# Optimization experiments

Hardware: AMD Instinct MI355X
Metric: run time of the kernel (lower is better)

## Reference

```python
import jax, jax.numpy as jnp
import numpy as np

EPS_BN = 1e-4


def gcn_conv(x, W, b, src, dst):
    """PyG GCNConv with added self-loops and symmetric normalization."""
    N = x.shape[0]
    h = x @ W  # [N, out]
    # degree over targets, +1 for the implicit self-loop on every node
    deg = jnp.zeros((N,), x.dtype).at[dst].add(1.0) + 1.0
    dinv = jax.lax.rsqrt(deg)  # deg^{-1/2}
    norm = dinv[src] * dinv[dst]  # per-edge coefficient
    msg = h[src] * norm[:, None]  # [E, out] gather (memory-bound)
    out = jax.ops.segment_sum(msg, dst, num_segments=N)
    out = out + h * (dinv * dinv)[:, None]  # self-loop term, norm = 1/deg
    return out + b


def batch_norm(x, gamma, beta):
    # training-mode BN over the node dim, biased variance (matches torch train)
    m = jnp.mean(x, axis=0)
    v = jnp.mean(jnp.square(x - m), axis=0)
    return (x - m) * jax.lax.rsqrt(v + EPS_BN) * gamma + beta


def setup_inputs() -> dict:
    key = jax.random.key(0)
    ks = jax.random.split(key, 8)
    N, E, D = 100000, 1600000, 64
    L = 2
    x = jax.random.normal(ks[0], (N, D), jnp.float32)
    edge_index = jax.random.randint(ks[1], (2, E), 0, N, jnp.int32)
    batch = jnp.sort(jax.random.randint(ks[2], (N,), 0, 128, jnp.int32))
    s = 1.0 / np.sqrt(D)
    return {
        "x": x,
        "edge_index": edge_index,
        "batch": batch,
        "enc_W": jax.random.normal(ks[3], (L, D, D), jnp.float32) * s,
        "enc_b": jnp.zeros((L, D), jnp.float32),
        "enc_gamma": jnp.ones((L, D), jnp.float32),
        "enc_beta": jnp.zeros((L, D), jnp.float32),
        "attr_W": jax.random.normal(ks[4], (L, D, D), jnp.float32) * s,
        "attr_b": jnp.zeros((L, D), jnp.float32),
        "attr_gamma": jnp.ones((L, D), jnp.float32),
        "attr_beta": jnp.zeros((L, D), jnp.float32),
        "str_W": jax.random.normal(ks[5], (L, D, D), jnp.float32) * s,
        "str_b": jnp.zeros((L, D), jnp.float32),
        "str_gamma": jnp.ones((L, D), jnp.float32),
        "str_beta": jnp.zeros((L, D), jnp.float32),
    }


def reference(x, edge_index, batch, enc_W, enc_b, enc_gamma, enc_beta,
              attr_W, attr_b, attr_gamma, attr_beta,
              str_W, str_b, str_gamma, str_beta):
    src, dst = edge_index[0], edge_index[1]
    L = enc_W.shape[0]

    # ---- Encoder: GCN -> sigmoid -> (dropout id) -> BN ----
    h = x
    for i in range(L):
        h = gcn_conv(h, enc_W[i], enc_b[i], src, dst)
        h = jax.nn.sigmoid(h)
        h = batch_norm(h, enc_gamma[i], enc_beta[i])
    x_enc = h
    # x_pool = global_mean_pool(x_enc, batch) is computed but discarded upstream

    # ---- Attribute decoder: GCN -> (dropout) -> sigmoid (except last) -> BN ----
    h = x_enc
    for i in range(L):
        h = gcn_conv(h, attr_W[i], attr_b[i], src, dst)
        if i != L - 1:
            h = jax.nn.sigmoid(h)
        h = batch_norm(h, attr_gamma[i], attr_beta[i])
    x_att = h

    # ---- Structure decoder ----
    h = x_enc
    for i in range(L):
        h = gcn_conv(h, str_W[i], str_b[i], src, dst)
        if i != L - 1:
            h = jax.nn.sigmoid(h)
        else:
            h = jax.nn.sigmoid(h * 0.5)
        h = batch_norm(h, str_gamma[i], str_beta[i])
    x_str = h

    return (x_str, x_att, x_enc)
```

## Files before the change

kernel.cpp:

```cpp
#include <hip/hip_runtime.h>

#define D 64
#define BCH 4096

typedef __attribute__((ext_vector_type(8))) _Float16 f16x8;
typedef __attribute__((ext_vector_type(4))) float f32x4;

__device__ __forceinline__ float sigmoidf_(float x) {
    return 1.0f / (1.0f + __expf(-x));
}
__device__ __forceinline__ float h2f(ushort u) {
    _Float16 h;
    __builtin_memcpy(&h, &u, 2);
    return (float)h;
}
__device__ __forceinline__ ushort f2h(float f) {
    _Float16 h = (_Float16)f;
    ushort u;
    __builtin_memcpy(&u, &h, 2);
    return u;
}
__device__ __forceinline__ float2 up2(uint v) {
    float2 r;
    r.x = h2f((ushort)(v & 0xffffu));
    r.y = h2f((ushort)(v >> 16));
    return r;
}


__global__ __launch_bounds__(256) void bin_edges(const int* __restrict__ src,
                                                 const int* __restrict__ dst,
                                                 int* __restrict__ bcur,
                                                 uint* __restrict__ bins,
                                                 int CAP, int E) {
    __shared__ uint lp[BCH];
    __shared__ unsigned char lb[BCH];
    __shared__ int hist[128], base[128];
    int t = threadIdx.x;
    int e0 = blockIdx.x * BCH;
    if (t < 128) hist[t] = 0;
    __syncthreads();
    for (int k = t; k < BCH; k += 256) {
        int e = e0 + k;
        uint p = 0xFFFFFFFFu;
        int b = 0;
        if (e < E) {
            int s_ = src[e];
            int d_ = dst[e];
            b = d_ >> 10;
            atomicAdd(&hist[b], 1);
            p = ((uint)s_ << 10) | (uint)(d_ & 1023);
        }
        lp[k] = p;
        lb[k] = (unsigned char)b;
    }
    __syncthreads();
    if (t < 128) {
        int c = hist[t];
        base[t] = (c > 0) ? atomicAdd(&bcur[t], c) : 0;
        hist[t] = 0;
    }
    __syncthreads();
    for (int k = t; k < BCH; k += 256) {
        uint p = lp[k];
        if (p != 0xFFFFFFFFu) {
            int b = lb[k];
            int pos = base[b] + atomicAdd(&hist[b], 1);
            bins[(size_t)b * CAP + pos] = p;
        }
    }
}

__global__ __launch_bounds__(128) void scan_nb(const int* __restrict__ bcur,
                                               int* __restrict__ boff,
                                               int* __restrict__ csr,
                                               int NB, int N, int E) {
    __shared__ int tmp[128];
    int t = threadIdx.x;
    int v = (t < NB) ? bcur[t] : 0;
    tmp[t] = v;
    __syncthreads();
    for (int o = 1; o < 128; o <<= 1) {
        int x = (t >= o) ? tmp[t - o] : 0;
        __syncthreads();
        tmp[t] += x;
        __syncthreads();
    }
    if (t < NB) boff[t] = tmp[t] - v;
    if (t == 0) csr[N] = E;
}

__global__ __launch_bounds__(256) void build_csr(const uint* __restrict__ bins,
                                                 const int* __restrict__ bcur,
                                                 const int* __restrict__ boff,
                                                 int* __restrict__ csr,
                                                 int* __restrict__ sorted,
                                                 float* __restrict__ dinv,
                                                 float* __restrict__ rdinv,
                                                 int CAP, int N) {
    __shared__ int hist[1024];
    __shared__ int part[256];
    int t = threadIdx.x;
    int b = blockIdx.x;
    int nb0 = b << 10;
    int cnt = bcur[b];
    int e0 = boff[b];
    const uint* bp = bins + (size_t)b * CAP;
    for (int k = t; k < 1024; k += 256) hist[k] = 0;
    __syncthreads();
    for (int k = t; k < cnt; k += 256) atomicAdd(&hist[bp[k] & 1023u], 1);
    __syncthreads();
    int v0 = hist[4 * t], v1 = hist[4 * t + 1], v2 = hist[4 * t + 2], v3 = hist[4 * t + 3];
    part[t] = v0 + v1 + v2 + v3;
    __syncthreads();
    for (int o = 1; o < 256; o <<= 1) {
        int x = (t >= o) ? part[t - o] : 0;
        __syncthreads();
        part[t] += x;
        __syncthreads();
    }
    int run = (t > 0) ? part[t - 1] : 0;
    int pre[4];
    pre[0] = run;
    pre[1] = run + v0;
    pre[2] = run + v0 + v1;
    pre[3] = run + v0 + v1 + v2;
    int deg[4] = {v0, v1, v2, v3};
    __syncthreads();
    hist[4 * t + 0] = e0 + pre[0];
    hist[4 * t + 1] = e0 + pre[1];
    hist[4 * t + 2] = e0 + pre[2];
    hist[4 * t + 3] = e0 + pre[3];
#pragma unroll
    for (int j = 0; j < 4; j++) {
        int node = nb0 + 4 * t + j;
        if (node < N) {
            csr[node] = e0 + pre[j];
            float c = (float)deg[j] + 1.0f;
            dinv[node] = rsqrtf(c);
            rdinv[node] = sqrtf(c);
        }
    }
    __syncthreads();
    for (int k = t; k < cnt; k += 256) {
        uint p = bp[k];
        int pos = atomicAdd(&hist[p & 1023u], 1);
        sorted[pos] = (int)(p >> 10);
    }
}


__global__ __launch_bounds__(256) void prep_xd(const float* __restrict__ x,
                                               const float* __restrict__ dinv,
                                               ushort* __restrict__ actd, int N16) {
    int p = blockIdx.x * 256 + threadIdx.x;
    if (p >= N16) return;
    int n = p >> 4;
    float d = dinv[n];
    float4 v = reinterpret_cast<const float4*>(x)[p];
    ushort4 o;
    o.x = f2h(v.x * d);
    o.y = f2h(v.y * d);
    o.z = f2h(v.z * d);
    o.w = f2h(v.w * d);
    reinterpret_cast<ushort4*>(actd)[p] = o;
}

__global__ __launch_bounds__(256) void wprep(const float* __restrict__ W,
                                             ushort* __restrict__ wfrag) {
    int idx = blockIdx.x * 256 + threadIdx.x;
    if (idx >= 4096) return;
    int i = idx & 7;
    int lane = (idx >> 3) & 63;
    int hc = idx >> 9;
    int h = hc >> 2, c = hc & 3;
    int k = h * 32 + (lane >> 4) * 8 + i;
    int j = c * 16 + (lane & 15);
    wfrag[idx] = f2h(W[k * 64 + j]);
}

__global__ __launch_bounds__(256) void layer_prep(const float* __restrict__ ssum,
                                                  const float* __restrict__ sssq,
                                                  const float* __restrict__ gamma,
                                                  const float* __restrict__ beta,
                                                  const float* __restrict__ W,
                                                  float* __restrict__ A,
                                                  float* __restrict__ C,
                                                  float* __restrict__ u,
                                                  ushort* __restrict__ wfrag,
                                                  float invN) {
    __shared__ float As[64], Cs[64];
    int t = threadIdx.x;
    if (t < 64) {
        float m = ssum[t] * invN;
        float var = sssq[t] * invN - m * m;
        float rs = rsqrtf(var + 1e-4f);
        float a = rs * gamma[t];
        As[t] = a;
        A[t] = a;
        float c = fmaf(-m, a, beta[t]);
        Cs[t] = c;
        C[t] = c;
    }
    __syncthreads();
    if (t < 64) {
        float s = 0.f;
        for (int k = 0; k < 64; k++) s = fmaf(Cs[k], W[k * 64 + t], s);
        u[t] = s;
    }
    for (int idx = t; idx < 4096; idx += 256) {
        int i = idx & 7;
        int lane = (idx >> 3) & 63;
        int hc = idx >> 9;
        int h = hc >> 2, c = hc & 3;
        int k = h * 32 + (lane >> 4) * 8 + i;
        int j = c * 16 + (lane & 15);
        wfrag[idx] = f2h(W[k * 64 + j] * As[k]);
    }
}

__global__ __launch_bounds__(64) void finalize_aff(const float* __restrict__ ssum,
                                                   const float* __restrict__ sssq,
                                                   const float* __restrict__ gamma,
                                                   const float* __restrict__ beta,
                                                   float* __restrict__ A,
                                                   float* __restrict__ C, float invN) {
    int c = threadIdx.x;
    float m = ssum[c] * invN;
    float var = sssq[c] * invN - m * m;
    float rs = rsqrtf(var + 1e-4f);
    float a = rs * gamma[c];
    A[c] = a;
    C[c] = fmaf(-m, a, beta[c]);
}


__global__ __launch_bounds__(256) void agg_g(const ushort* __restrict__ actd,
                                             const int* __restrict__ ptr,
                                             const int* __restrict__ srcs,
                                             const float* __restrict__ dinv,
                                             const float* __restrict__ rdinv,
                                             ushort* __restrict__ zh,
                                             float* __restrict__ ssum,
                                             float* __restrict__ sssq,
                                             float* __restrict__ qout, int N, int E) {
    __shared__ float red[2][4][64];
    int lane = threadIdx.x & 63;
    int wv = threadIdx.x >> 6;
    int l7 = lane & 7;
    int Em1 = E - 1;
    const bool do_stats = (ssum != nullptr);
    const bool do_q = (qout != nullptr);
    float ps = 0.f, pq = 0.f;
    int Nh = (N + 1) >> 1;
    for (int n0 = blockIdx.x * 4 + wv; n0 < Nh; n0 += gridDim.x * 4) {
        int nA = n0;
        int nB = n0 + Nh;
        bool hasB = nB < N;
        int sA = ptr[nA], eA = ptr[nA + 1];
        int sB = 0, eB = 0;
        if (hasB) { sB = ptr[nB]; eB = ptr[nB + 1]; }
        float selfA = h2f(actd[((size_t)nA << 6) + lane]);
        float accA = selfA;
        float dnA = dinv[nA];
        float accB = 0.f, dnB = 0.f;
        if (hasB) {
            float selfB = h2f(actd[((size_t)nB << 6) + lane]);
            accB = selfB;
            dnB = dinv[nB];
            if (do_stats) {
                float rb = rdinv[nB];
                float b = selfB * rb;
                ps += b;
                pq += b * b;
            }
        }
        if (do_stats) {
            float ra = rdinv[nA];
            float a = selfA * ra;
            ps += a;
            pq += a * a;
        }
        float qaA = 0.f, qaB = 0.f;
        int iA = sA, iB = sB;
        int idxA = srcs[min(iA + l7, Em1)];
        int idxB = hasB ? srcs[min(iB + l7, Em1)] : 0;
        while (iA + 8 <= eA || iB + 8 <= eB) {
            bool gA = iA + 8 <= eA;
            bool gB = iB + 8 <= eB;
            ushort ua[8], ub[8];
            if (gA) {
#pragma unroll
                for (int j = 0; j < 8; j++) {
                    int u = __builtin_amdgcn_readlane(idxA, j);
                    ua[j] = actd[((size_t)u << 6) + lane];
                    if (do_q) qaA += dinv[u];
                }
            }
            if (gB) {
#pragma unroll
                for (int j = 0; j < 8; j++) {
                    int u = __builtin_amdgcn_readlane(idxB, j);
                    ub[j] = actd[((size_t)u << 6) + lane];
                    if (do_q) qaB += dinv[u];
                }
            }
            int idxA2 = idxA, idxB2 = idxB;
            if (gA) idxA2 = srcs[min(iA + 8 + l7, Em1)];
            if (gB) idxB2 = srcs[min(iB + 8 + l7, Em1)];
            if (gA) {
                accA += ((h2f(ua[0]) + h2f(ua[1])) + (h2f(ua[2]) + h2f(ua[3]))) +
                        ((h2f(ua[4]) + h2f(ua[5])) + (h2f(ua[6]) + h2f(ua[7])));
                iA += 8;
                idxA = idxA2;
            }
            if (gB) {
                accB += ((h2f(ub[0]) + h2f(ub[1])) + (h2f(ub[2]) + h2f(ub[3]))) +
                        ((h2f(ub[4]) + h2f(ub[5])) + (h2f(ub[6]) + h2f(ub[7])));
                iB += 8;
                idxB = idxB2;
            }
        }
        if (iA < eA) {
#pragma unroll
            for (int j = 0; j < 8; j++) {
                int u = __builtin_amdgcn_readlane(idxA, j);
                float w = (iA + j < eA) ? 1.0f : 0.0f;
                float f = h2f(actd[((size_t)u << 6) + lane]);
                accA = fmaf(w, f, accA);
                if (do_q) qaA = fmaf(w, dinv[u], qaA);
            }
        }
        if (hasB && iB < eB) {
#pragma unroll
            for (int j = 0; j < 8; j++) {
                int u = __builtin_amdgcn_readlane(idxB, j);
                float w = (iB + j < eB) ? 1.0f : 0.0f;
                float f = h2f(actd[((size_t)u << 6) + lane]);
                accB = fmaf(w, f, accB);
                if (do_q) qaB = fmaf(w, dinv[u], qaB);
            }
        }
        if (do_q && lane == 0) {
            qout[nA] = dnA * (dnA + qaA);
            if (hasB) qout[nB] = dnB * (dnB + qaB);
        }
        zh[((size_t)nA << 6) + lane] = f2h(accA * dnA);
        if (hasB) zh[((size_t)nB << 6) + lane] = f2h(accB * dnB);
    }
    if (do_stats) {
        red[0][wv][lane] = ps;
        red[1][wv][lane] = pq;
        __syncthreads();
        if (wv == 0) {
            float t0 = red[0][0][lane] + red[0][1][lane] + red[0][2][lane] + red[0][3][lane];
            float t1 = red[1][0][lane] + red[1][1][lane] + red[1][2][lane] + red[1][3][lane];
            atomicAdd(&ssum[lane], t0);
            atomicAdd(&sssq[lane], t1);
        }
    }
}

__global__ __launch_bounds__(256) void agg_dual(const ushort* __restrict__ ab,
                                                const int* __restrict__ ptr,
                                                const int* __restrict__ srcs,
                                                const float* __restrict__ dinv,
                                                const float* __restrict__ rdinv,
                                                ushort* __restrict__ zab,
                                                float* __restrict__ ssA,
                                                float* __restrict__ sqA,
                                                float* __restrict__ ssS,
                                                float* __restrict__ sqS,
                                                int N, int E) {
    __shared__ float red[2][4][128];
    int lane = threadIdx.x & 63;
    int wv = threadIdx.x >> 6;
    int l7 = lane & 7;
    int Em1 = E - 1;
    float2 ps = make_float2(0.f, 0.f), pq = make_float2(0.f, 0.f);
    int Nh = (N + 1) >> 1;
    for (int n0 = blockIdx.x * 4 + wv; n0 < Nh; n0 += gridDim.x * 4) {
        int nA = n0;
        int nB = n0 + Nh;
        bool hasB = nB < N;
        int sA = ptr[nA], eA = ptr[nA + 1];
        int sB = 0, eB = 0;
        if (hasB) { sB = ptr[nB]; eB = ptr[nB + 1]; }
        uint suA = *reinterpret_cast<const uint*>(ab + ((size_t)nA << 7) + (lane << 1));
        float2 accA = up2(suA);
        float dnA = dinv[nA];
        {
            float r = rdinv[nA];
            float ax = accA.x * r, ay = accA.y * r;
            ps.x += ax; ps.y += ay;
            pq.x += ax * ax; pq.y += ay * ay;
        }
        float2 accB = make_float2(0.f, 0.f);
        float dnB = 0.f;
        if (hasB) {
            uint suB = *reinterpret_cast<const uint*>(ab + ((size_t)nB << 7) + (lane << 1));
            accB = up2(suB);
            dnB = dinv[nB];
            float r = rdinv[nB];
            float ax = accB.x * r, ay = accB.y * r;
            ps.x += ax; ps.y += ay;
            pq.x += ax * ax; pq.y += ay * ay;
        }
        int iA = sA, iB = sB;
        int idxA = srcs[min(iA + l7, Em1)];
        int idxB = hasB ? srcs[min(iB + l7, Em1)] : 0;
        while (iA + 8 <= eA || iB + 8 <= eB) {
            bool gA = iA + 8 <= eA;
            bool gB = iB + 8 <= eB;
            uint va[8], vb[8];
            if (gA) {
#pragma unroll
                for (int j = 0; j < 8; j++) {
                    int u = __builtin_amdgcn_readlane(idxA, j);
                    va[j] = *reinterpret_cast<const uint*>(ab + ((size_t)u << 7) + (lane << 1));
                }
            }
            if (gB) {
#pragma unroll
                for (int j = 0; j < 8; j++) {
                    int u = __builtin_amdgcn_readlane(idxB, j);
                    vb[j] = *reinterpret_cast<const uint*>(ab + ((size_t)u << 7) + (lane << 1));
                }
            }
            int idxA2 = idxA, idxB2 = idxB;
            if (gA) idxA2 = srcs[min(iA + 8 + l7, Em1)];
            if (gB) idxB2 = srcs[min(iB + 8 + l7, Em1)];
            if (gA) {
#pragma unroll
                for (int j = 0; j < 8; j++) {
                    float2 f = up2(va[j]);
                    accA.x += f.x;
                    accA.y += f.y;
                }
                iA += 8;
                idxA = idxA2;
            }
            if (gB) {
#pragma unroll
                for (int j = 0; j < 8; j++) {
                    float2 f = up2(vb[j]);
                    accB.x += f.x;
                    accB.y += f.y;
                }
                iB += 8;
                idxB = idxB2;
            }
        }
        if (iA < eA) {
#pragma unroll
            for (int j = 0; j < 8; j++) {
                int u = __builtin_amdgcn_readlane(idxA, j);
                uint v = *reinterpret_cast<const uint*>(ab + ((size_t)u << 7) + (lane << 1));
                float w = (iA + j < eA) ? 1.0f : 0.0f;
                float2 f = up2(v);
                accA.x = fmaf(w, f.x, accA.x);
                accA.y = fmaf(w, f.y, accA.y);
            }
        }
        if (hasB && iB < eB) {
#pragma unroll
            for (int j = 0; j < 8; j++) {
                int u = __builtin_amdgcn_readlane(idxB, j);
                uint v = *reinterpret_cast<const uint*>(ab + ((size_t)u << 7) + (lane << 1));
                float w = (iB + j < eB) ? 1.0f : 0.0f;
                float2 f = up2(v);
                accB.x = fmaf(w, f.x, accB.x);
                accB.y = fmaf(w, f.y, accB.y);
            }
        }
        uint pkA = (uint)f2h(accA.x * dnA) | ((uint)f2h(accA.y * dnA) << 16);
        *reinterpret_cast<uint*>(zab + ((size_t)nA << 7) + (lane << 1)) = pkA;
        if (hasB) {
            uint pkB = (uint)f2h(accB.x * dnB) | ((uint)f2h(accB.y * dnB) << 16);
            *reinterpret_cast<uint*>(zab + ((size_t)nB << 7) + (lane << 1)) = pkB;
        }
    }
    red[0][wv][2 * lane + 0] = ps.x;
    red[0][wv][2 * lane + 1] = ps.y;
    red[1][wv][2 * lane + 0] = pq.x;
    red[1][wv][2 * lane + 1] = pq.y;
    __syncthreads();
    if (wv == 0) {
#pragma unroll
        for (int m0 = 0; m0 < 2; m0++) {
            int m = lane + m0 * 64;
            float t0 = red[0][0][m] + red[0][1][m] + red[0][2][m] + red[0][3][m];
            float t1 = red[1][0][m] + red[1][1][m] + red[1][2][m] + red[1][3][m];
            if (m < 64) {
                atomicAdd(&ssA[m], t0);
                atomicAdd(&sqA[m], t1);
            } else {
                atomicAdd(&ssS[m - 64], t0);
                atomicAdd(&sqS[m - 64], t1);
            }
        }
    }
}

template <int MODE, bool HAS_AFF, int OM>
__global__ __launch_bounds__(256) void gemm_mfma(const ushort* __restrict__ zh, int is,
                                                 const ushort* __restrict__ wfrag,
                                                 const float* __restrict__ bias,
                                                 const float* __restrict__ u,
                                                 const float* __restrict__ q,
                                                 const float* __restrict__ dinv,
                                                 ushort* __restrict__ outh, int os,
                                                 float* __restrict__ outf,
                                                 float* __restrict__ s0,
                                                 float* __restrict__ s1, int N) {
    int tid = threadIdx.x;
    int lane = tid & 63;
    int wv = tid >> 6;
    int l15 = lane & 15;
    int lg = lane >> 4;
    int tb = blockIdx.x * 64;

    const ushort* zrow = zh + (size_t)(tb + wv * 16 + l15) * is + (lg << 3);
    f16x8 a0 = *reinterpret_cast<const f16x8*>(zrow);
    f16x8 a1 = *reinterpret_cast<const f16x8*>(zrow + 32);

    const f16x8* wf = reinterpret_cast<const f16x8*>(wfrag) + lane;

    f32x4 acc[4];
#pragma unroll
    for (int c = 0; c < 4; c++) {
        f32x4 t = {0.f, 0.f, 0.f, 0.f};
        t = __builtin_amdgcn_mfma_f32_16x16x32_f16(a0, wf[(0 * 4 + c) * 64], t, 0, 0, 0);
        t = __builtin_amdgcn_mfma_f32_16x16x32_f16(a1, wf[(1 * 4 + c) * 64], t, 0, 0, 0);
        acc[c] = t;
    }

    int rowbase = tb + wv * 16 + lg * 4;
    float qv[4], dv[4];
    bool vld[4];
#pragma unroll
    for (int r = 0; r < 4; r++) {
        int row = rowbase + r;
        vld[r] = row < N;
        qv[r] = (HAS_AFF && vld[r]) ? q[row] : 0.f;
        dv[r] = (OM == 0 && vld[r]) ? dinv[row] : 0.f;
    }
    float sa[4], sq[4];
#pragma unroll
    for (int c = 0; c < 4; c++) { sa[c] = 0.f; sq[c] = 0.f; }

#pragma unroll
    for (int c = 0; c < 4; c++) {
        int col = c * 16 + l15;
        float bcol = bias[col];
        float ucol = HAS_AFF ? u[col] : 0.f;
        float Acol = (OM == 2) ? s0[col] : 0.f;
        float Ccol = (OM == 2) ? s1[col] : 0.f;
#pragma unroll
        for (int r = 0; r < 4; r++) {
            if (!vld[r]) continue;
            float o = acc[c][r] + bcol;
            if (HAS_AFF) o = fmaf(qv[r], ucol, o);
            float a = (MODE == 0) ? sigmoidf_(o)
                                  : ((MODE == 1) ? o : sigmoidf_(0.5f * o));
            int row = rowbase + r;
            if (OM == 0) {
                outh[(size_t)row * os + col] = f2h(a * dv[r]);
            } else if (OM == 1) {
                sa[c] += a;
                sq[c] += a * a;
            } else {
                outf[((size_t)row << 6) + col] = fmaf(a, Acol, Ccol);
            }
        }
    }

    if (OM == 1) {
        __shared__ float red[2][4][4][16];
#pragma unroll
        for (int c = 0; c < 4; c++) {
            sa[c] += __shfl_xor(sa[c], 16);
            sa[c] += __shfl_xor(sa[c], 32);
            sq[c] += __shfl_xor(sq[c], 16);
            sq[c] += __shfl_xor(sq[c], 32);
        }
        if (lg == 0) {
#pragma unroll
            for (int c = 0; c < 4; c++) {
                red[0][wv][c][l15] = sa[c];
                red[1][wv][c][l15] = sq[c];
            }
        }
        __syncthreads();
        if (wv == 0) {
            int c = lane >> 4, l = lane & 15;
            float t0 = red[0][0][c][l] + red[0][1][c][l] + red[0][2][c][l] + red[0][3][c][l];
            float t1 = red[1][0][c][l] + red[1][1][c][l] + red[1][2][c][l] + red[1][3][c][l];
            atomicAdd(&s0[lane], t0);
            atomicAdd(&s1[lane], t1);
        }
    }
}

__global__ __launch_bounds__(256) void gemm_dual(const ushort* __restrict__ zh,
                                                 const ushort* __restrict__ wfA,
                                                 const ushort* __restrict__ wfS,
                                                 const float* __restrict__ bA,
                                                 const float* __restrict__ bS,
                                                 const float* __restrict__ uA,
                                                 const float* __restrict__ uS,
                                                 const float* __restrict__ q,
                                                 const float* __restrict__ dinv,
                                                 ushort* __restrict__ outAB, int N) {
    int tid = threadIdx.x;
    int lane = tid & 63;
    int wv = tid >> 6;
    int l15 = lane & 15;
    int lg = lane >> 4;
    int tb = blockIdx.x * 64;

    const ushort* zrow = zh + ((size_t)(tb + wv * 16 + l15) << 6) + (lg << 3);
    f16x8 a0 = *reinterpret_cast<const f16x8*>(zrow);
    f16x8 a1 = *reinterpret_cast<const f16x8*>(zrow + 32);

    const f16x8* wa = reinterpret_cast<const f16x8*>(wfA) + lane;
    const f16x8* wsp = reinterpret_cast<const f16x8*>(wfS) + lane;

    f32x4 accA[4], accS[4];
#pragma unroll
    for (int c = 0; c < 4; c++) {
        f32x4 t = {0.f, 0.f, 0.f, 0.f};
        t = __builtin_amdgcn_mfma_f32_16x16x32_f16(a0, wa[(0 * 4 + c) * 64], t, 0, 0, 0);
        t = __builtin_amdgcn_mfma_f32_16x16x32_f16(a1, wa[(1 * 4 + c) * 64], t, 0, 0, 0);
        accA[c] = t;
        f32x4 t2 = {0.f, 0.f, 0.f, 0.f};
        t2 = __builtin_amdgcn_mfma_f32_16x16x32_f16(a0, wsp[(0 * 4 + c) * 64], t2, 0, 0, 0);
        t2 = __builtin_amdgcn_mfma_f32_16x16x32_f16(a1, wsp[(1 * 4 + c) * 64], t2, 0, 0, 0);
        accS[c] = t2;
    }

    int rowbase = tb + wv * 16 + lg * 4;
    float qv[4], dv[4];
    bool vld[4];
#pragma unroll
    for (int r = 0; r < 4; r++) {
        int row = rowbase + r;
        vld[r] = row < N;
        qv[r] = vld[r] ? q[row] : 0.f;
        dv[r] = vld[r] ? dinv[row] : 0.f;
    }
#pragma unroll
    for (int c = 0; c < 4; c++) {
        int col = c * 16 + l15;
        float bcA = bA[col], ucA = uA[col];
        float bcS = bS[col], ucS = uS[col];
#pragma unroll
        for (int r = 0; r < 4; r++) {
            if (!vld[r]) continue;
            int row = rowbase + r;
            float oA = fmaf(qv[r], ucA, accA[c][r] + bcA);
            float oS = fmaf(qv[r], ucS, accS[c][r] + bcS);
            float aA = sigmoidf_(oA);
            float aS = sigmoidf_(oS);
            outAB[((size_t)row << 7) + col] = f2h(aA * dv[r]);
            outAB[((size_t)row << 7) + 64 + col] = f2h(aS * dv[r]);
        }
    }
}

__global__ __launch_bounds__(256) void bn_apply_h(const ushort* __restrict__ actd,
                                                  const float* __restrict__ rdinv,
                                                  const float* __restrict__ A,
                                                  const float* __restrict__ C,
                                                  float* __restrict__ out, int N16) {
    int p = blockIdx.x * 256 + threadIdx.x;
    if (p >= N16) return;
    int n = p >> 4;
    int cb = (p & 15) * 4;
    float r = rdinv[n];
    ushort4 v = reinterpret_cast<const ushort4*>(actd)[p];
    float4 o;
    o.x = fmaf(h2f(v.x) * r, A[cb + 0], C[cb + 0]);
    o.y = fmaf(h2f(v.y) * r, A[cb + 1], C[cb + 1]);
    o.z = fmaf(h2f(v.z) * r, A[cb + 2], C[cb + 2]);
    o.w = fmaf(h2f(v.w) * r, A[cb + 3], C[cb + 3]);
    reinterpret_cast<float4*>(out)[p] = o;
}


extern "C" void kernel_launch(void* const* d_in, const int* in_sizes, int n_in,
                              void* d_out, int out_size, void* d_ws, size_t ws_size,
                              hipStream_t stream) {
    const int N = in_sizes[0] / D;
    const int E = in_sizes[1] / 2;

    const float* x = (const float*)d_in[0];
    const int* ei = (const int*)d_in[1];
    const int* src_in = ei;
    const int* dst_in = ei + E;
    const float* encW = (const float*)d_in[3];
    const float* encb = (const float*)d_in[4];
    const float* encg = (const float*)d_in[5];
    const float* encbe = (const float*)d_in[6];
    const float* attW = (const float*)d_in[7];
    const float* attb = (const float*)d_in[8];
    const float* attg = (const float*)d_in[9];
    const float* attbe = (const float*)d_in[10];
    const float* strW = (const float*)d_in[11];
    const float* strb = (const float*)d_in[12];
    const float* strg = (const float*)d_in[13];
    const float* strbe = (const float*)d_in[14];

    const int NB = (N + 1023) >> 10;
    int CAP = (E + NB - 1) / NB;
    CAP = CAP + CAP / 8 + 256;
    CAP = (CAP + 255) & ~255;

    char* ws = (char*)d_ws;
    size_t off = 0;
    auto alloc = [&](size_t bytes) -> char* {
        char* p = ws + off;
        off += (bytes + 255) & ~(size_t)255;
        return p;
    };
    int* csr = (int*)alloc((size_t)(N + 1) * 4);
    int* bcur = (int*)alloc(128 * 4);
    int* boff = (int*)alloc(128 * 4);
    float* dinv = (float*)alloc((size_t)N * 4);
    float* rdinv = (float*)alloc((size_t)N * 4);
    float* q = (float*)alloc((size_t)N * 4);
    float* stats = (float*)alloc(6 * 128 * 4);
    float* aff = (float*)alloc(6 * 128 * 4);
    float* ubuf = (float*)alloc(6 * 64 * 4);
    ushort* wf = (ushort*)alloc(6 * 4096 * 2);
    int* sorted = (int*)alloc((size_t)E * 4);
    ushort* zh = (ushort*)alloc((size_t)(N + 64) * 64 * 2);
    size_t binbytes = (size_t)NB * CAP * 4;
    size_t zabbytes = (size_t)(N + 64) * 128 * 2;
    char* region = alloc(binbytes > zabbytes ? binbytes : zabbytes);
    uint* bins = (uint*)region;
    ushort* zab = (ushort*)region;
    ushort* hA = (ushort*)alloc((size_t)N * 64 * 2);
    ushort* hB = (ushort*)alloc((size_t)N * 64 * 2);
    ushort* hAB = (ushort*)alloc((size_t)(N + 64) * 128 * 2);

    float* out_str = (float*)d_out;
    float* out_att = out_str + (size_t)N * D;
    float* out_enc = out_att + (size_t)N * D;

    hipMemsetAsync(bcur, 0, 128 * 4, stream);
    hipMemsetAsync(stats, 0, 6 * 128 * 4, stream);

    int N16 = N * 16;
    int g16 = (N16 + 255) / 256;
    int gT = (N + 63) / 64;
    float invN = 1.0f / (float)N;

    float* A0 = aff + 0 * 128; float* C0 = A0 + 64;
    float* A1 = aff + 1 * 128; float* C1 = A1 + 64;
    float* A2 = aff + 2 * 128; float* C2 = A2 + 64;
    float* A3 = aff + 3 * 128; float* C3 = A3 + 64;
    float* A4 = aff + 4 * 128; float* C4 = A4 + 64;
    float* A5 = aff + 5 * 128; float* C5 = A5 + 64;
    ushort* wf0 = wf + 0 * 4096;
    ushort* wf1 = wf + 1 * 4096;
    ushort* wf2 = wf + 2 * 4096;
    ushort* wf3 = wf + 3 * 4096;
    ushort* wf4 = wf + 4 * 4096;
    ushort* wf5 = wf + 5 * 4096;

    bin_edges<<<(E + BCH - 1) / BCH, 256, 0, stream>>>(src_in, dst_in, bcur,
                                                       bins, CAP, E);
    scan_nb<<<1, 128, 0, stream>>>(bcur, boff, csr, NB, N, E);
    build_csr<<<NB, 256, 0, stream>>>(bins, bcur, boff, csr, sorted,
                                      dinv, rdinv, CAP, N);

    prep_xd<<<g16, 256, 0, stream>>>(x, dinv, hA, N16);
    wprep<<<16, 256, 0, stream>>>(encW, wf0);
    agg_g<<<2048, 256, 0, stream>>>(hA, csr, sorted, dinv, rdinv, zh,
                                    nullptr, nullptr, q, N, E);
    gemm_mfma<0, false, 0><<<gT, 256, 0, stream>>>(zh, 64, wf0, encb, nullptr,
                                                   q, dinv, hB, 64, nullptr,
                                                   nullptr, nullptr, N);
    agg_g<<<2048, 256, 0, stream>>>(hB, csr, sorted, dinv, rdinv, zh,
                                    stats + 0, stats + 64, nullptr, N, E);
    layer_prep<<<1, 256, 0, stream>>>(stats + 0, stats + 64, encg, encbe,
                                      encW + 4096, A0, C0, ubuf + 0, wf1, invN);
    gemm_mfma<0, true, 0><<<gT, 256, 0, stream>>>(zh, 64, wf1, encb + 64, ubuf + 0,
                                                  q, dinv, hA, 64, nullptr,
                                                  nullptr, nullptr, N);
    agg_g<<<2048, 256, 0, stream>>>(hA, csr, sorted, dinv, rdinv, zh,
                                    stats + 128, stats + 192, nullptr, N, E);
    layer_prep<<<1, 256, 0, stream>>>(stats + 128, stats + 192, encg + 64,
                                      encbe + 64, attW, A1, C1, ubuf + 64, wf2, invN);
    layer_prep<<<1, 256, 0, stream>>>(stats + 128, stats + 192, encg + 64,
                                      encbe + 64, strW, A1, C1, ubuf + 128, wf3, invN);
    bn_apply_h<<<g16, 256, 0, stream>>>(hA, rdinv, A1, C1, out_enc, N16);
    gemm_dual<<<gT, 256, 0, stream>>>(zh, wf2, wf3, attb, strb, ubuf + 64,
                                      ubuf + 128, q, dinv, hAB, N);
    agg_dual<<<2048, 256, 0, stream>>>(hAB, csr, sorted, dinv, rdinv, zab,
                                       stats + 256, stats + 320,
                                       stats + 512, stats + 576, N, E);
    layer_prep<<<1, 256, 0, stream>>>(stats + 256, stats + 320, attg, attbe,
                                      attW + 4096, A2, C2, ubuf + 192, wf4, invN);
    gemm_mfma<1, true, 1><<<gT, 256, 0, stream>>>(zab, 128, wf4, attb + 64,
                                                  ubuf + 192, q, dinv, nullptr, 0,
                                                  nullptr, stats + 384, stats + 448, N);
    finalize_aff<<<1, 64, 0, stream>>>(stats + 384, stats + 448, attg + 64,
                                       attbe + 64, A3, C3, invN);
    gemm_mfma<1, true, 2><<<gT, 256, 0, stream>>>(zab, 128, wf4, attb + 64,
                                                  ubuf + 192, q, dinv, nullptr, 0,
                                                  out_att, A3, C3, N);
    layer_prep<<<1, 256, 0, stream>>>(stats + 512, stats + 576, strg, strbe,
                                      strW + 4096, A4, C4, ubuf + 320, wf5, invN);
    gemm_mfma<2, true, 1><<<gT, 256, 0, stream>>>(zab + 64, 128, wf5, strb + 64,
                                                  ubuf + 320, q, dinv, nullptr, 0,
                                                  nullptr, stats + 640, stats + 704, N);
    finalize_aff<<<1, 64, 0, stream>>>(stats + 640, stats + 704, strg + 64,
                                       strbe + 64, A5, C5, invN);
    gemm_mfma<2, true, 2><<<gT, 256, 0, stream>>>(zab + 64, 128, wf5, strb + 64,
                                                  ubuf + 320, q, dinv, nullptr, 0,
                                                  out_str, A5, C5, N);
}
```

Before: 602.8 us.

## Store final-layer activations in fp16 and apply BN elementwise; simplify agg_dual loop

The last attribute and structure GCN layers used to run the MFMA GEMM twice: once to gather BN statistics and once to recompute and write normalized outputs. The first pass now also writes the pre-BN activation as fp16, and a light elementwise kernel applies the BN affine from that buffer, removing the second GEMM. This adds an fp16 write and read round trip and rounds the final outputs through fp16 before normalization. Separately, agg_dual drops its two-nodes-per-wave interleaving and goes back to one node per wave, with the next index batch prefetched. That trades the extra parallelism in flight for simpler control flow.

```diff
diff --git a/kernel.cpp b/kernel.cpp
--- a/kernel.cpp
+++ b/kernel.cpp
@@ -378,107 +378,46 @@
     int l7 = lane & 7;
     int Em1 = E - 1;
     float2 ps = make_float2(0.f, 0.f), pq = make_float2(0.f, 0.f);
-    int Nh = (N + 1) >> 1;
-    for (int n0 = blockIdx.x * 4 + wv; n0 < Nh; n0 += gridDim.x * 4) {
-        int nA = n0;
-        int nB = n0 + Nh;
-        bool hasB = nB < N;
-        int sA = ptr[nA], eA = ptr[nA + 1];
-        int sB = 0, eB = 0;
-        if (hasB) { sB = ptr[nB]; eB = ptr[nB + 1]; }
-        uint suA = *reinterpret_cast<const uint*>(ab + ((size_t)nA << 7) + (lane << 1));
-        float2 accA = up2(suA);
-        float dnA = dinv[nA];
+    for (int n = blockIdx.x * 4 + wv; n < N; n += gridDim.x * 4) {
+        int s = ptr[n], e = ptr[n + 1];
+        uint su = *reinterpret_cast<const uint*>(ab + ((size_t)n << 7) + (lane << 1));
+        float2 acc = up2(su);
         {
-            float r = rdinv[nA];
-            float ax = accA.x * r, ay = accA.y * r;
+            float r = rdinv[n];
+            float ax = acc.x * r, ay = acc.y * r;
             ps.x += ax; ps.y += ay;
             pq.x += ax * ax; pq.y += ay * ay;
         }
-        float2 accB = make_float2(0.f, 0.f);
-        float dnB = 0.f;
-        if (hasB) {
-            uint suB = *reinterpret_cast<const uint*>(ab + ((size_t)nB << 7) + (lane << 1));
-            accB = up2(suB);
-            dnB = dinv[nB];
-            float r = rdinv[nB];
-            float ax = accB.x * r, ay = accB.y * r;
-            ps.x += ax; ps.y += ay;
-            pq.x += ax * ax; pq.y += ay * ay;
-        }
-        int iA = sA, iB = sB;
-        int idxA = srcs[min(iA + l7, Em1)];
-        int idxB = hasB ? srcs[min(iB + l7, Em1)] : 0;
-        while (iA + 8 <= eA || iB + 8 <= eB) {
-            bool gA = iA + 8 <= eA;
-            bool gB = iB + 8 <= eB;
-            uint va[8], vb[8];
-            if (gA) {
-#pragma unroll
-                for (int j = 0; j < 8; j++) {
-                    int u = __builtin_amdgcn_readlane(idxA, j);
-                    va[j] = *reinterpret_cast<const uint*>(ab + ((size_t)u << 7) + (lane << 1));
-                }
-            }
-            if (gB) {
-#pragma unroll
-                for (int j = 0; j < 8; j++) {
-                    int u = __builtin_amdgcn_readlane(idxB, j);
-                    vb[j] = *reinterpret_cast<const uint*>(ab + ((size_t)u << 7) + (lane << 1));
-                }
-            }
-            int idxA2 = idxA, idxB2 = idxB;
-            if (gA) idxA2 = srcs[min(iA + 8 + l7, Em1)];
-            if (gB) idxB2 = srcs[min(iB + 8 + l7, Em1)];
-            if (gA) {
-#pragma unroll
-                for (int j = 0; j < 8; j++) {
-                    float2 f = up2(va[j]);
-                    accA.x += f.x;
-                    accA.y += f.y;
-                }
-                iA += 8;
-                idxA = idxA2;
-            }
-            if (gB) {
-#pragma unroll
-                for (int j = 0; j < 8; j++) {
-                    float2 f = up2(vb[j]);
-                    accB.x += f.x;
-                    accB.y += f.y;
-                }
-                iB += 8;
-                idxB = idxB2;
-            }
-        }
-        if (iA < eA) {
+        int i = s;
+        int idx8 = srcs[min(i + l7, Em1)];
+        while (i + 8 <= e) {
+            int ni = i + 8;
+            int nidx = srcs[min(ni + l7, Em1)];
 #pragma unroll
             for (int j = 0; j < 8; j++) {
-                int u = __builtin_amdgcn_readlane(idxA, j);
+                int u = __builtin_amdgcn_readlane(idx8, j);
                 uint v = *reinterpret_cast<const uint*>(ab + ((size_t)u << 7) + (lane << 1));
-                float w = (iA + j < eA) ? 1.0f : 0.0f;
                 float2 f = up2(v);
-                accA.x = fmaf(w, f.x, accA.x);
-                accA.y = fmaf(w, f.y, accA.y);
-            }
-        }
-        if (hasB && iB < eB) {
+                acc.x += f.x;
+                acc.y += f.y;
+            }
+            idx8 = nidx;
+            i = ni;
+        }
+        if (i < e) {
 #pragma unroll
             for (int j = 0; j < 8; j++) {
-                int u = __builtin_amdgcn_readlane(idxB, j);
+                int u = __builtin_amdgcn_readlane(idx8, j);
                 uint v = *reinterpret_cast<const uint*>(ab + ((size_t)u << 7) + (lane << 1));
-                float w = (iB + j < eB) ? 1.0f : 0.0f;
+                float w = (i + j < e) ? 1.0f : 0.0f;
                 float2 f = up2(v);
-                accB.x = fmaf(w, f.x, accB.x);
-                accB.y = fmaf(w, f.y, accB.y);
-            }
-        }
-        uint pkA = (uint)f2h(accA.x * dnA) | ((uint)f2h(accA.y * dnA) << 16);
-        *reinterpret_cast<uint*>(zab + ((size_t)nA << 7) + (lane << 1)) = pkA;
-        if (hasB) {
-            uint pkB = (uint)f2h(accB.x * dnB) | ((uint)f2h(accB.y * dnB) << 16);
-            *reinterpret_cast<uint*>(zab + ((size_t)nB << 7) + (lane << 1)) = pkB;
-        }
+                acc.x = fmaf(w, f.x, acc.x);
+                acc.y = fmaf(w, f.y, acc.y);
+            }
+        }
+        float dn = dinv[n];
+        uint pk = (uint)f2h(acc.x * dn) | ((uint)f2h(acc.y * dn) << 16);
+        *reinterpret_cast<uint*>(zab + ((size_t)n << 7) + (lane << 1)) = pk;
     }
     red[0][wv][2 * lane + 0] = ps.x;
     red[0][wv][2 * lane + 1] = ps.y;
@@ -510,7 +449,6 @@
                                                  const float* __restrict__ q,
                                                  const float* __restrict__ dinv,
                                                  ushort* __restrict__ outh, int os,
-                                                 float* __restrict__ outf,
                                                  float* __restrict__ s0,
                                                  float* __restrict__ s1, int N) {
     int tid = threadIdx.x;
@@ -554,8 +492,6 @@
         int col = c * 16 + l15;
         float bcol = bias[col];
         float ucol = HAS_AFF ? u[col] : 0.f;
-        float Acol = (OM == 2) ? s0[col] : 0.f;
-        float Ccol = (OM == 2) ? s1[col] : 0.f;
 #pragma unroll
         for (int r = 0; r < 4; r++) {
             if (!vld[r]) continue;
@@ -566,11 +502,10 @@
             int row = rowbase + r;
             if (OM == 0) {
                 outh[(size_t)row * os + col] = f2h(a * dv[r]);
-            } else if (OM == 1) {
+            } else {
+                outh[(size_t)row * os + col] = f2h(a);
                 sa[c] += a;
                 sq[c] += a * a;
-            } else {
-                outf[((size_t)row << 6) + col] = fmaf(a, Acol, Ccol);
             }
         }
     }
@@ -684,6 +619,22 @@
     o.y = fmaf(h2f(v.y) * r, A[cb + 1], C[cb + 1]);
     o.z = fmaf(h2f(v.z) * r, A[cb + 2], C[cb + 2]);
     o.w = fmaf(h2f(v.w) * r, A[cb + 3], C[cb + 3]);
+    reinterpret_cast<float4*>(out)[p] = o;
+}
+
+__global__ __launch_bounds__(256) void bn_apply_hf(const ushort* __restrict__ acth,
+                                                   const float* __restrict__ A,
+                                                   const float* __restrict__ C,
+                                                   float* __restrict__ out, int N16) {
+    int p = blockIdx.x * 256 + threadIdx.x;
+    if (p >= N16) return;
+    int cb = (p & 15) * 4;
+    ushort4 v = reinterpret_cast<const ushort4*>(acth)[p];
+    float4 o;
+    o.x = fmaf(h2f(v.x), A[cb + 0], C[cb + 0]);
+    o.y = fmaf(h2f(v.y), A[cb + 1], C[cb + 1]);
+    o.z = fmaf(h2f(v.z), A[cb + 2], C[cb + 2]);
+    o.w = fmaf(h2f(v.w), A[cb + 3], C[cb + 3]);
     reinterpret_cast<float4*>(out)[p] = o;
 }
 
@@ -740,8 +691,8 @@
     char* region = alloc(binbytes > zabbytes ? binbytes : zabbytes);
     uint* bins = (uint*)region;
     ushort* zab = (ushort*)region;
-    ushort* hA = (ushort*)alloc((size_t)N * 64 * 2);
-    ushort* hB = (ushort*)alloc((size_t)N * 64 * 2);
+    ushort* hA = (ushort*)alloc((size_t)(N + 64) * 64 * 2);
+    ushort* hB = (ushort*)alloc((size_t)(N + 64) * 64 * 2);
     ushort* hAB = (ushort*)alloc((size_t)(N + 64) * 128 * 2);
 
     float* out_str = (float*)d_out;
@@ -780,14 +731,14 @@
     agg_g<<<2048, 256, 0, stream>>>(hA, csr, sorted, dinv, rdinv, zh,
                                     nullptr, nullptr, q, N, E);
     gemm_mfma<0, false, 0><<<gT, 256, 0, stream>>>(zh, 64, wf0, encb, nullptr,
-                                                   q, dinv, hB, 64, nullptr,
+                                                   q, dinv, hB, 64,
                                                    nullptr, nullptr, N);
     agg_g<<<2048, 256, 0, stream>>>(hB, csr, sorted, dinv, rdinv, zh,
                                     stats + 0, stats + 64, nullptr, N, E);
     layer_prep<<<1, 256, 0, stream>>>(stats + 0, stats + 64, encg, encbe,
                                       encW + 4096, A0, C0, ubuf + 0, wf1, invN);
     gemm_mfma<0, true, 0><<<gT, 256, 0, stream>>>(zh, 64, wf1, encb + 64, ubuf + 0,
-                                                  q, dinv, hA, 64, nullptr,
+                                                  q, dinv, hA, 64,
                                                   nullptr, nullptr, N);
     agg_g<<<2048, 256, 0, stream>>>(hA, csr, sorted, dinv, rdinv, zh,
                                     stats + 128, stats + 192, nullptr, N, E);
@@ -804,21 +755,17 @@
     layer_prep<<<1, 256, 0, stream>>>(stats + 256, stats + 320, attg, attbe,
                                       attW + 4096, A2, C2, ubuf + 192, wf4, invN);
     gemm_mfma<1, true, 1><<<gT, 256, 0, stream>>>(zab, 128, wf4, attb + 64,
-                                                  ubuf + 192, q, dinv, nullptr, 0,
-                                                  nullptr, stats + 384, stats + 448, N);
+                                                  ubuf + 192, q, dinv, hAB, 64,
+                                                  stats + 384, stats + 448, N);
     finalize_aff<<<1, 64, 0, stream>>>(stats + 384, stats + 448, attg + 64,
                                        attbe + 64, A3, C3, invN);
-    gemm_mfma<1, true, 2><<<gT, 256, 0, stream>>>(zab, 128, wf4, attb + 64,
-                                                  ubuf + 192, q, dinv, nullptr, 0,
-                                                  out_att, A3, C3, N);
+    bn_apply_hf<<<g16, 256, 0, stream>>>(hAB, A3, C3, out_att, N16);
     layer_prep<<<1, 256, 0, stream>>>(stats + 512, stats + 576, strg, strbe,
                                       strW + 4096, A4, C4, ubuf + 320, wf5, invN);
     gemm_mfma<2, true, 1><<<gT, 256, 0, stream>>>(zab + 64, 128, wf5, strb + 64,
-                                                  ubuf + 320, q, dinv, nullptr, 0,
-                                                  nullptr, stats + 640, stats + 704, N);
+                                                  ubuf + 320, q, dinv, hA, 64,
+                                                  stats + 640, stats + 704, N);
     finalize_aff<<<1, 64, 0, stream>>>(stats + 640, stats + 704, strg + 64,
                                        strbe + 64, A5, C5, invN);
-    gemm_mfma<2, true, 2><<<gT, 256, 0, stream>>>(zab + 64, 128, wf5, strb + 64,
-                                                  ubuf + 320, q, dinv, nullptr, 0,
-                                                  out_str, A5, C5, N);
-}
+    bn_apply_hf<<<g16, 256, 0, stream>>>(hA, A5, C5, out_str, N16);
+}
```

Result: no change. 595.3 us (-1.3%).
